# Kernel tuning notes

Hardware: AMD Instinct MI355X
Metric: run time of the kernel (lower is better)

## Reference

```python
import jax, jax.numpy as jnp
import numpy as np

H = 1024  # hidden_size


def _cell(x, W, b):
    # x: [S, B, D_in]; W: [4H, D_in]; b: [4H]
    # One big batched matmul over all timesteps (no recurrence exists).
    gates = jnp.einsum('sbd,gd->sbg', x, W) + b  # [S, B, 4H]
    i, f, g, o = jnp.split(gates, 4, axis=-1)
    i = jax.nn.sigmoid(i)
    g = jnp.tanh(g)
    o = jax.nn.sigmoid(o)
    c = i * g
    h = o * jnp.tanh(c)
    return h, c


def setup_inputs() -> dict:
    key = jax.random.key(0)
    ks = jax.random.split(key, 9)
    S, B, D = 2048, 8, 1024
    s = 1.0 / np.sqrt(D)
    s2 = 1.0 / np.sqrt(2 * H)
    return {
        'x': jax.random.normal(ks[0], (S, B, D), dtype=jnp.float32),
        'W_f0': jax.random.uniform(ks[1], (4 * H, D), jnp.float32, -s, s),
        'b_f0': jax.random.uniform(ks[2], (4 * H,), jnp.float32, -s, s),
        'W_b0': jax.random.uniform(ks[3], (4 * H, D), jnp.float32, -s, s),
        'b_b0': jax.random.uniform(ks[4], (4 * H,), jnp.float32, -s, s),
        'W_f1': jax.random.uniform(ks[5], (4 * H, 2 * H), jnp.float32, -s2, s2),
        'b_f1': jax.random.uniform(ks[6], (4 * H,), jnp.float32, -s2, s2),
        'W_b1': jax.random.uniform(ks[7], (4 * H, 2 * H), jnp.float32, -s2, s2),
        'b_b1': jax.random.uniform(ks[8], (4 * H,), jnp.float32, -s2, s2),
    }


def reference(x, W_f0, b_f0, W_b0, b_b0, W_f1, b_f1, W_b1, b_b1):
    out = x
    h_ns, c_ns = [], []
    for (Wf, bf, Wb, bb) in [(W_f0, b_f0, W_b0, b_b0), (W_f1, b_f1, W_b1, b_b1)]:
        h_f, c_f = _cell(out, Wf, bf)  # forward direction
        h_b, c_b = _cell(out, Wb, bb)  # backward direction (same per-t math)
        out = jnp.concatenate([h_f, h_b], axis=-1)  # [S, B, 2H]
        # forward final state is at t = S-1; backward final state at t = 0
        h_ns += [h_f[-1], h_b[0]]
        c_ns += [c_f[-1], c_b[0]]
    h_n = jnp.stack(h_ns, axis=0)  # [num_layers*2, B, H]
    c_n = jnp.stack(c_ns, axis=0)
    return out, h_n, c_n
```

## Files before the change

### kernel.cpp

```cpp
#include <hip/hip_runtime.h>
#include <hip/hip_bf16.h>

#define S_LEN 2048
#define BATCH 8
#define HID   1024
#define NP    3072
#define MROWS 16384

using bf16x8 = __attribute__((ext_vector_type(8))) short;
using f32x4  = __attribute__((ext_vector_type(4))) float;

__device__ __forceinline__ unsigned short f2b(float f) {
  unsigned int u = __builtin_bit_cast(unsigned int, f);
  u += 0x7fffu + ((u >> 16) & 1u);
  return (unsigned short)(u >> 16);
}

__device__ __forceinline__ float sigf(float x) {
  return 1.f / (1.f + __expf(-x));
}
__device__ __forceinline__ float tanh_f(float x) {
  return 2.f / (1.f + __expf(-2.f * x)) - 1.f;
}

__device__ __forceinline__ void load_lds16(const void* g, void* l) {
  __builtin_amdgcn_global_load_lds(
      (const __attribute__((address_space(1))) void*)g,
      (__attribute__((address_space(3))) void*)(unsigned int)(unsigned long long)l,
      16, 0, 0);
}

#define MEMFENCE asm volatile("" ::: "memory")
#define BARRIER  do { MEMFENCE; __builtin_amdgcn_s_barrier(); MEMFENCE; } while (0)

__device__ __forceinline__ void permute_w_dev(const float* __restrict__ W,
                                              unsigned short* __restrict__ Wp,
                                              long id, int K) {
  const long i = id * 4;
  const int np = (int)(i / K);
  const int k0 = (int)(i % K);
  const int chunk = np / 48, rem = np % 48;
  const int g3 = rem >> 4, hl = rem & 15;
  const int og = (g3 == 0) ? 0 : (g3 == 1) ? 2 : 3;
  const int n  = og * 1024 + chunk * 16 + hl;
  const float4 v = *reinterpret_cast<const float4*>(W + (long)n * K + k0);
  ushort4 u;
  u.x = f2b(v.x); u.y = f2b(v.y); u.z = f2b(v.z); u.w = f2b(v.w);
  *reinterpret_cast<ushort4*>(Wp + i) = u;
}

__global__ void prep(const float* __restrict__ x, unsigned short* __restrict__ x_bf,
                     const float* __restrict__ Wf0, const float* __restrict__ Wb0,
                     const float* __restrict__ Wf1, const float* __restrict__ Wb1,
                     unsigned short* __restrict__ pf0, unsigned short* __restrict__ pb0,
                     unsigned short* __restrict__ pf1, unsigned short* __restrict__ pb1,
                     const float* __restrict__ bf0, const float* __restrict__ bb0,
                     const float* __restrict__ bf1, const float* __restrict__ bb1,
                     float* __restrict__ bpf0, float* __restrict__ bpb0,
                     float* __restrict__ bpf1, float* __restrict__ bpb1) {
  const int blk = blockIdx.x;
  const int tid = threadIdx.x;
  if (blk < 16384) {
    const int i = blk * 256 + tid;
    const float4 v = reinterpret_cast<const float4*>(x)[i];
    ushort4 u;
    u.x = f2b(v.x); u.y = f2b(v.y); u.z = f2b(v.z); u.w = f2b(v.w);
    reinterpret_cast<ushort4*>(x_bf)[i] = u;
  } else if (blk < 19456) {
    permute_w_dev(Wf0, pf0, (long)(blk - 16384) * 256 + tid, 1024);
  } else if (blk < 22528) {
    permute_w_dev(Wb0, pb0, (long)(blk - 19456) * 256 + tid, 1024);
  } else if (blk < 28672) {
    permute_w_dev(Wf1, pf1, (long)(blk - 22528) * 256 + tid, 2048);
  } else if (blk < 34816) {
    permute_w_dev(Wb1, pb1, (long)(blk - 28672) * 256 + tid, 2048);
  } else {
    const int r = blk - 34816;
    const int which = r / 12;
    const int np = (r % 12) * 256 + tid;
    const float* bs = which == 0 ? bf0 : which == 1 ? bb0 : which == 2 ? bf1 : bb1;
    float* bd       = which == 0 ? bpf0 : which == 1 ? bpb0 : which == 2 ? bpf1 : bpb1;
    const int chunk = np / 48, rem = np % 48;
    const int g3 = rem >> 4, hl = rem & 15;
    const int og = (g3 == 0) ? 0 : (g3 == 1) ? 2 : 3;
    bd[np] = bs[og * 1024 + chunk * 16 + hl];
  }
}

template <int MODE>
__global__ void __launch_bounds__(256, 2)
lstm_gemm(const unsigned short* __restrict__ A,
          const unsigned short* __restrict__ WpF,
          const unsigned short* __restrict__ WpB,
          const float* __restrict__ bpF, const float* __restrict__ bpB,
          int K,
          unsigned short* __restrict__ out_bf, float* __restrict__ out_f,
          float* __restrict__ hn, float* __restrict__ cn) {
  __shared__ __align__(16) char lds[81920];

  const int dir = blockIdx.z;
  const unsigned short* __restrict__ Wp = dir ? WpB : WpF;
  const float* __restrict__ bp = dir ? bpB : bpF;

  const int f    = blockIdx.x + (blockIdx.y << 4);
  const int virt = (f >> 3) + (f & 7) * 256;
  const int bm   = virt >> 4;
  const int bn   = virt & 15;

  const int tid  = threadIdx.x;
  const int wid  = tid >> 6;
  const int lane = tid & 63;
  const int wm   = wid >> 1;
  const int wn   = wid & 1;

  const int  nt = K >> 6;
  const long K2 = (long)K * 2;

  const int rlane = lane >> 3;
  const int cb    = (((lane & 7) ^ rlane) << 4);
  const char* Asrc = (const char*)A  + ((long)bm * 128 + rlane) * K2 + cb;
  const char* Bsrc = (const char*)Wp + ((long)bn * 192 + rlane) * K2 + cb;

  const int l15 = lane & 15;
  const int hi  = lane >> 4;
  const int c0  = ((hi ^ (l15 & 7)) << 4);
  const int aro = (wm * 64 + l15) * 128;
  const int bro = 16384 + (wn * 96 + l15) * 128;

  f32x4 acc[4][6];
  const f32x4 zero = {0.f, 0.f, 0.f, 0.f};
#pragma unroll
  for (int i = 0; i < 4; ++i)
#pragma unroll
    for (int j = 0; j < 6; ++j) acc[i][j] = zero;

  auto STAGE = [&](int t) {
    if (t >= nt) return;
    char* d = lds + (t & 1) * 40960;
    const long off = (long)t * 128;
#pragma unroll
    for (int s = 0; s < 4; ++s) {
      const int slot = s * 4 + wid;
      load_lds16(Asrc + (long)(slot * 8) * K2 + off, d + slot * 1024);
    }
#pragma unroll
    for (int s = 0; s < 6; ++s) {
      const int slot = s * 4 + wid;
      load_lds16(Bsrc + (long)(slot * 8) * K2 + off, d + 16384 + slot * 1024);
    }
  };

  STAGE(0);
  asm volatile("s_waitcnt vmcnt(0)" ::: "memory");
  BARRIER;

  for (int t = 0; t < nt; ++t) {
    STAGE(t + 1);

    const char* buf = lds + (t & 1) * 40960;
    bf16x8 a[4][2], b[6][2];
#pragma unroll
    for (int nf = 0; nf < 6; ++nf) {
      b[nf][0] = *(const bf16x8*)(buf + bro + nf * 2048 + c0);
      b[nf][1] = *(const bf16x8*)(buf + bro + nf * 2048 + (c0 ^ 64));
    }
#pragma unroll
    for (int mf = 0; mf < 4; ++mf) {
      a[mf][0] = *(const bf16x8*)(buf + aro + mf * 2048 + c0);
      a[mf][1] = *(const bf16x8*)(buf + aro + mf * 2048 + (c0 ^ 64));
    }

    __builtin_amdgcn_s_setprio(1);
#pragma unroll
    for (int mf = 0; mf < 4; ++mf)
#pragma unroll
      for (int nf = 0; nf < 6; ++nf) {
        acc[mf][nf] = __builtin_amdgcn_mfma_f32_16x16x32_bf16(
            a[mf][0], b[nf][0], acc[mf][nf], 0, 0, 0);
        acc[mf][nf] = __builtin_amdgcn_mfma_f32_16x16x32_bf16(
            a[mf][1], b[nf][1], acc[mf][nf], 0, 0, 0);
      }
    __builtin_amdgcn_s_setprio(0);

    asm volatile("s_waitcnt vmcnt(0)" ::: "memory");
    BARRIER;
  }

  const int col    = l15;
  const int rbase  = hi * 4;
  const int chunk0 = bn * 4 + wn * 2;
  const int Lidx   = MODE * 2 + dir;

#pragma unroll
  for (int hg = 0; hg < 2; ++hg) {
    const int chunk  = chunk0 + hg;
    const int h      = chunk * 16 + col;
    const int outcol = dir * HID + h;
    const float bi = bp[chunk * 48 + col];
    const float bg = bp[chunk * 48 + 16 + col];
    const float bo = bp[chunk * 48 + 32 + col];
#pragma unroll
    for (int mf = 0; mf < 4; ++mf) {
#pragma unroll
      for (int r = 0; r < 4; ++r) {
        const int m = bm * 128 + wm * 64 + mf * 16 + rbase + r;
        const float iv = acc[mf][hg * 3 + 0][r] + bi;
        const float gv = acc[mf][hg * 3 + 1][r] + bg;
        const float ov = acc[mf][hg * 3 + 2][r] + bo;
        const float is = sigf(iv);
        const float gt = tanh_f(gv);
        const float os = sigf(ov);
        const float c  = is * gt;
        const float hv = os * tanh_f(c);
        if (MODE == 0) {
          out_bf[(long)m * 2048 + outcol] = f2b(hv);
        } else {
          out_f[(long)m * 2048 + outcol] = hv;
        }
        const bool wst = (dir == 0) ? (m >= (S_LEN - 1) * BATCH) : (m < BATCH);
        if (wst) {
          const int b = (dir == 0) ? (m - (S_LEN - 1) * BATCH) : m;
          hn[((long)Lidx * BATCH + b) * HID + h] = hv;
          cn[((long)Lidx * BATCH + b) * HID + h] = c;
        }
      }
    }
  }
}

extern "C" void kernel_launch(void* const* d_in, const int* in_sizes, int n_in,
                              void* d_out, int out_size, void* d_ws, size_t ws_size,
                              hipStream_t stream) {
  const float* x    = (const float*)d_in[0];
  const float* W_f0 = (const float*)d_in[1];
  const float* b_f0 = (const float*)d_in[2];
  const float* W_b0 = (const float*)d_in[3];
  const float* b_b0 = (const float*)d_in[4];
  const float* W_f1 = (const float*)d_in[5];
  const float* b_f1 = (const float*)d_in[6];
  const float* W_b1 = (const float*)d_in[7];
  const float* b_b1 = (const float*)d_in[8];

  float* out = (float*)d_out;
  float* hn  = out + (long)MROWS * 2048;
  float* cn  = hn + 4 * BATCH * HID;

  unsigned short* x_bf  = (unsigned short*)d_ws;
  unsigned short* out1  = x_bf + (long)MROWS * 1024;
  unsigned short* wp_f0 = out1 + (long)MROWS * 2048;
  unsigned short* wp_b0 = wp_f0 + (long)NP * 1024;
  unsigned short* wp_f1 = wp_b0 + (long)NP * 1024;
  unsigned short* wp_b1 = wp_f1 + (long)NP * 2048;
  float* bp_f0 = (float*)(wp_b1 + (long)NP * 2048);
  float* bp_b0 = bp_f0 + NP;
  float* bp_f1 = bp_b0 + NP;
  float* bp_b1 = bp_f1 + NP;

  prep<<<34864, 256, 0, stream>>>(x, x_bf, W_f0, W_b0, W_f1, W_b1,
                                  wp_f0, wp_b0, wp_f1, wp_b1,
                                  b_f0, b_b0, b_f1, b_b1,
                                  bp_f0, bp_b0, bp_f1, bp_b1);

  dim3 grid(16, 128, 2);
  lstm_gemm<0><<<grid, 256, 0, stream>>>(x_bf, wp_f0, wp_b0, bp_f0, bp_b0, 1024,
                                         out1, nullptr, hn, cn);
  lstm_gemm<1><<<grid, 256, 0, stream>>>(out1, wp_f1, wp_b1, bp_f1, bp_b1, 2048,
                                         nullptr, out, hn, cn);
}
```

Before: 650.2 us.

## Widen GEMM tile to 128x384 with K-step 32 and drop block swizzle

Each block now computes a 128x384 output tile (12 N-fragments per wave) instead of 128x192, with the K-step per stage halved to 32 so LDS use drops to 64KB double-buffered. The grid halves in the N dimension, and the XCD-aware block remapping is replaced by a direct blockIdx mapping. The goal is more A-tile reuse per block and fewer blocks. The cost is 48 accumulator vectors per wave, which raises register pressure and may reduce occupancy, plus twice as many barrier iterations. Losing the swizzle may also hurt L2 locality.

```diff
diff --git a/kernel.cpp b/kernel.cpp
--- a/kernel.cpp
+++ b/kernel.cpp
@@ -96,16 +96,13 @@
           int K,
           unsigned short* __restrict__ out_bf, float* __restrict__ out_f,
           float* __restrict__ hn, float* __restrict__ cn) {
-  __shared__ __align__(16) char lds[81920];
+  __shared__ __align__(16) char lds[65536];
 
   const int dir = blockIdx.z;
   const unsigned short* __restrict__ Wp = dir ? WpB : WpF;
   const float* __restrict__ bp = dir ? bpB : bpF;
-
-  const int f    = blockIdx.x + (blockIdx.y << 4);
-  const int virt = (f >> 3) + (f & 7) * 256;
-  const int bm   = virt >> 4;
-  const int bn   = virt & 15;
+  const int bn = blockIdx.x;
+  const int bm = blockIdx.y;
 
   const int tid  = threadIdx.x;
   const int wid  = tid >> 6;
@@ -113,87 +110,86 @@
   const int wm   = wid >> 1;
   const int wn   = wid & 1;
 
-  const int  nt = K >> 6;
+  const int  nt = K >> 5;
   const long K2 = (long)K * 2;
 
-  const int rlane = lane >> 3;
-  const int cb    = (((lane & 7) ^ rlane) << 4);
-  const char* Asrc = (const char*)A  + ((long)bm * 128 + rlane) * K2 + cb;
-  const char* Bsrc = (const char*)Wp + ((long)bn * 192 + rlane) * K2 + cb;
+  const int rl = lane >> 2;
+  const int sg = ((lane & 3) ^ (rl & 3)) << 4;
+  const char* sA0 = (const char*)A  + ((long)bm * 128 + wid * 16      + rl) * K2 + sg;
+  const char* sA1 = (const char*)A  + ((long)bm * 128 + wid * 16 + 64 + rl) * K2 + sg;
+  const char* sB0 = (const char*)Wp + ((long)bn * 384 + wid * 16      + rl) * K2 + sg;
+  const int dA0 = wid * 1024;
+  const int dA1 = (wid + 4) * 1024;
+  const int dB0 = 8192 + wid * 1024;
+
+#define ISSUE(T) do {                                              \
+    char* d_ = lds + ((T) & 1) * 32768;                            \
+    const long ko_ = (long)(T) * 64;                               \
+    load_lds16(sA0 + ko_, d_ + dA0);                               \
+    load_lds16(sA1 + ko_, d_ + dA1);                               \
+    load_lds16(sB0 + ko_,                 d_ + dB0);               \
+    load_lds16(sB0 + ko_ +  64 * K2,      d_ + dB0 + 4096);        \
+    load_lds16(sB0 + ko_ + 128 * K2,      d_ + dB0 + 8192);        \
+    load_lds16(sB0 + ko_ + 192 * K2,      d_ + dB0 + 12288);       \
+    load_lds16(sB0 + ko_ + 256 * K2,      d_ + dB0 + 16384);       \
+    load_lds16(sB0 + ko_ + 320 * K2,      d_ + dB0 + 20480);       \
+  } while (0)
 
   const int l15 = lane & 15;
   const int hi  = lane >> 4;
-  const int c0  = ((hi ^ (l15 & 7)) << 4);
-  const int aro = (wm * 64 + l15) * 128;
-  const int bro = 16384 + (wn * 96 + l15) * 128;
-
-  f32x4 acc[4][6];
+  const int sb  = ((hi ^ (l15 & 3)) << 4);
+  const int aro = (wm * 64 + l15) * 64;
+  const int bro = 8192 + (wn * 192 + l15) * 64;
+
+  f32x4 acc[4][12];
   const f32x4 zero = {0.f, 0.f, 0.f, 0.f};
 #pragma unroll
   for (int i = 0; i < 4; ++i)
 #pragma unroll
-    for (int j = 0; j < 6; ++j) acc[i][j] = zero;
-
-  auto STAGE = [&](int t) {
-    if (t >= nt) return;
-    char* d = lds + (t & 1) * 40960;
-    const long off = (long)t * 128;
-#pragma unroll
-    for (int s = 0; s < 4; ++s) {
-      const int slot = s * 4 + wid;
-      load_lds16(Asrc + (long)(slot * 8) * K2 + off, d + slot * 1024);
-    }
-#pragma unroll
-    for (int s = 0; s < 6; ++s) {
-      const int slot = s * 4 + wid;
-      load_lds16(Bsrc + (long)(slot * 8) * K2 + off, d + 16384 + slot * 1024);
-    }
-  };
-
-  STAGE(0);
+    for (int j = 0; j < 12; ++j) acc[i][j] = zero;
+
+  ISSUE(0);
   asm volatile("s_waitcnt vmcnt(0)" ::: "memory");
   BARRIER;
 
+#pragma unroll 1
   for (int t = 0; t < nt; ++t) {
-    STAGE(t + 1);
-
-    const char* buf = lds + (t & 1) * 40960;
-    bf16x8 a[4][2], b[6][2];
-#pragma unroll
-    for (int nf = 0; nf < 6; ++nf) {
-      b[nf][0] = *(const bf16x8*)(buf + bro + nf * 2048 + c0);
-      b[nf][1] = *(const bf16x8*)(buf + bro + nf * 2048 + (c0 ^ 64));
+    if (t + 1 < nt) { ISSUE(t + 1); }
+
+    const char* buf = lds + (t & 1) * 32768;
+    bf16x8 a[4];
+#pragma unroll
+    for (int mf = 0; mf < 4; ++mf)
+      a[mf] = *(const bf16x8*)(buf + aro + mf * 1024 + sb);
+
+#pragma unroll
+    for (int g = 0; g < 3; ++g) {
+      bf16x8 b[4];
+#pragma unroll
+      for (int j = 0; j < 4; ++j)
+        b[j] = *(const bf16x8*)(buf + bro + (g * 4 + j) * 1024 + sb);
+      __builtin_amdgcn_s_setprio(1);
+#pragma unroll
+      for (int mf = 0; mf < 4; ++mf)
+#pragma unroll
+        for (int j = 0; j < 4; ++j)
+          acc[mf][g * 4 + j] = __builtin_amdgcn_mfma_f32_16x16x32_bf16(
+              a[mf], b[j], acc[mf][g * 4 + j], 0, 0, 0);
+      __builtin_amdgcn_s_setprio(0);
     }
-#pragma unroll
-    for (int mf = 0; mf < 4; ++mf) {
-      a[mf][0] = *(const bf16x8*)(buf + aro + mf * 2048 + c0);
-      a[mf][1] = *(const bf16x8*)(buf + aro + mf * 2048 + (c0 ^ 64));
-    }
-
-    __builtin_amdgcn_s_setprio(1);
-#pragma unroll
-    for (int mf = 0; mf < 4; ++mf)
-#pragma unroll
-      for (int nf = 0; nf < 6; ++nf) {
-        acc[mf][nf] = __builtin_amdgcn_mfma_f32_16x16x32_bf16(
-            a[mf][0], b[nf][0], acc[mf][nf], 0, 0, 0);
-        acc[mf][nf] = __builtin_amdgcn_mfma_f32_16x16x32_bf16(
-            a[mf][1], b[nf][1], acc[mf][nf], 0, 0, 0);
-      }
-    __builtin_amdgcn_s_setprio(0);
 
     asm volatile("s_waitcnt vmcnt(0)" ::: "memory");
     BARRIER;
   }
-
-  const int col    = l15;
-  const int rbase  = hi * 4;
-  const int chunk0 = bn * 4 + wn * 2;
-  const int Lidx   = MODE * 2 + dir;
-
-#pragma unroll
-  for (int hg = 0; hg < 2; ++hg) {
-    const int chunk  = chunk0 + hg;
+#undef ISSUE
+
+  const int col   = l15;
+  const int rbase = hi * 4;
+  const int Lidx  = MODE * 2 + dir;
+
+#pragma unroll
+  for (int c = 0; c < 4; ++c) {
+    const int chunk  = bn * 8 + wn * 4 + c;
     const int h      = chunk * 16 + col;
     const int outcol = dir * HID + h;
     const float bi = bp[chunk * 48 + col];
@@ -204,14 +200,14 @@
 #pragma unroll
       for (int r = 0; r < 4; ++r) {
         const int m = bm * 128 + wm * 64 + mf * 16 + rbase + r;
-        const float iv = acc[mf][hg * 3 + 0][r] + bi;
-        const float gv = acc[mf][hg * 3 + 1][r] + bg;
-        const float ov = acc[mf][hg * 3 + 2][r] + bo;
+        const float iv = acc[mf][c * 3 + 0][r] + bi;
+        const float gv = acc[mf][c * 3 + 1][r] + bg;
+        const float ov = acc[mf][c * 3 + 2][r] + bo;
         const float is = sigf(iv);
         const float gt = tanh_f(gv);
         const float os = sigf(ov);
-        const float c  = is * gt;
-        const float hv = os * tanh_f(c);
+        const float cc = is * gt;
+        const float hv = os * tanh_f(cc);
         if (MODE == 0) {
           out_bf[(long)m * 2048 + outcol] = f2b(hv);
         } else {
@@ -221,7 +217,7 @@
         if (wst) {
           const int b = (dir == 0) ? (m - (S_LEN - 1) * BATCH) : m;
           hn[((long)Lidx * BATCH + b) * HID + h] = hv;
-          cn[((long)Lidx * BATCH + b) * HID + h] = c;
+          cn[((long)Lidx * BATCH + b) * HID + h] = cc;
         }
       }
     }
@@ -261,7 +257,7 @@
                                   b_f0, b_b0, b_f1, b_b1,
                                   bp_f0, bp_b0, bp_f1, bp_b1);
 
-  dim3 grid(16, 128, 2);
+  dim3 grid(8, 128, 2);
   lstm_gemm<0><<<grid, 256, 0, stream>>>(x_bf, wp_f0, wp_b0, bp_f0, bp_b0, 1024,
                                          out1, nullptr, hn, cn);
   lstm_gemm<1><<<grid, 256, 0, stream>>>(out1, wp_f1, wp_b1, bp_f1, bp_b1, 2048,
```

Measured after the change: 675.5 us. +3.9%, slower.
